# Kernel tuning notes

Hardware: AMD Instinct MI355X
Metric: run time of the kernel (lower is better)

The kernel has to match this reference:

```python
import jax, jax.numpy as jnp
import numpy as np
import math

HEADS = 16
DIMS = 1024
SEQ_LEN = 2048
RANK_K = 128
BATCH = 8


def setup_inputs() -> dict:
    key = jax.random.key(0)
    ks = jax.random.split(key, 14)
    dh_std = 1.0 / math.sqrt(DIMS)
    proj_std = 1.0 / math.sqrt(RANK_K)
    inp = {
        "q": jax.random.normal(ks[0], (BATCH, SEQ_LEN, DIMS), jnp.float32),
        "k": jax.random.normal(ks[1], (BATCH, SEQ_LEN, DIMS), jnp.float32),
        "v": jax.random.normal(ks[2], (BATCH, SEQ_LEN, DIMS), jnp.float32),
        # nn.Linear weights [out, in], bias [out]
        "Wq": jax.random.uniform(ks[3], (DIMS, DIMS), jnp.float32, -dh_std, dh_std),
        "bq": jax.random.uniform(ks[4], (DIMS,), jnp.float32, -dh_std, dh_std),
        "Wk": jax.random.uniform(ks[5], (DIMS, DIMS), jnp.float32, -dh_std, dh_std),
        "bk": jax.random.uniform(ks[6], (DIMS,), jnp.float32, -dh_std, dh_std),
        "Wv": jax.random.uniform(ks[7], (DIMS, DIMS), jnp.float32, -dh_std, dh_std),
        "bv": jax.random.uniform(ks[8], (DIMS,), jnp.float32, -dh_std, dh_std),
        # Linformer low-rank projections [seq_length, k], uniform(-1/sqrt(k), 1/sqrt(k))
        "proj_k": jax.random.uniform(ks[9], (SEQ_LEN, RANK_K), jnp.float32, -proj_std, proj_std),
        "proj_v": jax.random.uniform(ks[10], (SEQ_LEN, RANK_K), jnp.float32, -proj_std, proj_std),
        "Wo": jax.random.uniform(ks[11], (DIMS, DIMS), jnp.float32, -dh_std, dh_std),
        "bo": jax.random.uniform(ks[12], (DIMS,), jnp.float32, -dh_std, dh_std),
    }
    return inp


def reference(q, k, v, Wq, bq, Wk, bk, Wv, bv, proj_k, proj_v, Wo, bo):
    B, N, D = q.shape
    H = HEADS
    dh = D // H
    Kr = proj_k.shape[1]

    kp = k @ Wk.T + bk                       # [B, N, D]
    # faithful to original: plain reshape (view), NOT a head-split transpose
    qp = (q @ Wq.T + bq).reshape(B, H, N, dh)  # [B, H, N, dh]
    vp = v @ Wv.T + bv                       # [B, N, D]

    pk = jnp.einsum('bnd,nk->bkd', kp, proj_k[:N])  # [B, Kr, D]
    pv = jnp.einsum('bnd,nk->bkd', vp, proj_v[:N])  # [B, Kr, D]
    pk = pk.reshape(B, Kr, H, dh).transpose(0, 2, 1, 3)  # [B, H, Kr, dh]
    pv = pv.reshape(B, Kr, H, dh).transpose(0, 2, 1, 3)  # [B, H, Kr, dh]

    # scores [B,H,N,Kr] -> transposed to [B,H,Kr,N]; softmax over N (seq) axis
    scores = jnp.einsum('bhnd,bhkd->bhkn', qp, pk) / math.sqrt(dh)
    attn = jax.nn.softmax(scores, axis=-1)   # [B, H, Kr, N]
    out = jnp.einsum('bhkn,bhkd->bhnd', attn, pv)  # [B, H, N, dh]
    out = out.transpose(0, 2, 1, 3).reshape(B, N, D)
    return out @ Wo.T + bo
```

## Files before the change

kernel.cpp:

```cpp
#include <hip/hip_runtime.h>

typedef unsigned short u16;
typedef unsigned int   u32;
typedef __attribute__((ext_vector_type(4))) float fx4;
typedef __attribute__((ext_vector_type(8))) __bf16 bf16x8;
typedef __attribute__((ext_vector_type(8))) unsigned short us8;
typedef __attribute__((ext_vector_type(2))) unsigned int u32x2;

__device__ __forceinline__ u16 f2bf(float x){
  u32 u = __builtin_bit_cast(u32, x);
  u += 0x7fffu + ((u >> 16) & 1u);
  return (u16)(u >> 16);
}
__device__ __forceinline__ float b2f(u16 h){
  u32 u = ((u32)h) << 16;
  return __builtin_bit_cast(float, u);
}
__device__ __forceinline__ void gld16(const void* g, void* l){
  __builtin_amdgcn_global_load_lds(
      (const __attribute__((address_space(1))) u32*)g,
      (__attribute__((address_space(3))) u32*)l, 16, 0, 0);
}
__device__ __forceinline__ void xcd_remap(u32& bx, u32& by, u32& bz){
  u32 nx = gridDim.x, ny = gridDim.y, nz = gridDim.z;
  u32 nwg = nx * ny * nz;
  u32 orig = (blockIdx.z * ny + blockIdx.y) * nx + blockIdx.x;
  u32 lid = (orig & 7u) * (nwg >> 3) + (orig >> 3);
  bx = lid % nx;
  u32 rem = lid / nx;
  by = rem % ny;
  bz = rem / ny;
}

__global__ __launch_bounds__(256) void k_f2bf(const float* __restrict__ in,
                                              u16* __restrict__ out, int n8){
  int i = blockIdx.x * 256 + threadIdx.x;
  const int stride = gridDim.x * 256;
  for (; i < n8; i += stride){
    const float4* p = (const float4*)in + (long)i * 2;
    float4 a = p[0], b = p[1];
    us8 o = { f2bf(a.x), f2bf(a.y), f2bf(a.z), f2bf(a.w),
              f2bf(b.x), f2bf(b.y), f2bf(b.z), f2bf(b.w) };
    *((us8*)out + i) = o;
  }
}

__global__ __launch_bounds__(256) void k_f2bfW(const float* __restrict__ w0,
                                               const float* __restrict__ w1,
                                               const float* __restrict__ w2,
                                               const float* __restrict__ w3,
                                               u16* __restrict__ out){
  const float* src = blockIdx.y == 0 ? w0 : blockIdx.y == 1 ? w1 :
                     blockIdx.y == 2 ? w2 : w3;
  u16* dst = out + (long)blockIdx.y * 1048576;
  int i = blockIdx.x * 256 + threadIdx.x;
  const int stride = gridDim.x * 256;
  for (; i < 131072; i += stride){
    const float4* p = (const float4*)src + (long)i * 2;
    float4 a = p[0], b = p[1];
    us8 o = { f2bf(a.x), f2bf(a.y), f2bf(a.z), f2bf(a.w),
              f2bf(b.x), f2bf(b.y), f2bf(b.z), f2bf(b.w) };
    *((us8*)dst + i) = o;
  }
}

__global__ void k_zero(float* p, int n){
  int i = blockIdx.x * 256 + threadIdx.x;
  if (i < n) p[i] = 0.f;
}

__global__ __launch_bounds__(256) void k_tconv(const float* __restrict__ in,
                                               u16* __restrict__ out,
                                               int R, int C, long sIn, long sOut,
                                               float* __restrict__ colsum){
  in  += (long)blockIdx.z * sIn;
  out += (long)blockIdx.z * sOut;
  const int c0 = blockIdx.x * 64, r0 = blockIdx.y * 64;
  __shared__ u16 tile[64][66];
  __shared__ float red[256];
  const int t = threadIdx.x;
  const int cc = t & 63, wq = t >> 6;
  float part = 0.f;
  #pragma unroll
  for (int i = 0; i < 16; ++i){
    int rr = i * 4 + wq;
    float v = in[(long)(r0 + rr) * C + c0 + cc];
    tile[rr][cc] = f2bf(v);
    part += v;
  }
  if (colsum){
    red[t] = part;
    __syncthreads();
    if (t < 64){
      float s = red[t] + red[t + 64] + red[t + 128] + red[t + 192];
      atomicAdd(&colsum[c0 + t], s);
    }
  }
  __syncthreads();
  const int oc0 = t >> 5, jb = (t & 31) * 2;
  #pragma unroll
  for (int i = 0; i < 8; ++i){
    int oc = oc0 + i * 8;
    u32 pk2 = (u32)tile[jb][oc] | ((u32)tile[jb + 1][oc] << 16);
    *(u32*)(out + (long)(c0 + oc) * R + r0 + jb) = pk2;
  }
}

template<int BM, int BN, int MODE, int EPI, typename OutT>
__global__ __launch_bounds__(256) void k_gemm(
    const u16* __restrict__ A, int lda, long sAz,
    const u16* __restrict__ B, int ldb, long sBz,
    OutT* __restrict__ C, int ldc, long sCz,
    int K, const float* __restrict__ bias, const float* __restrict__ srow, float scale)
{
  constexpr int BK = 64;
  constexpr int FM = BM / 32, FN = BN / 32;
  __shared__ u16 ldsA[BM * BK];
  __shared__ u16 ldsB[BN * BK];
  u32 bx, by, bz;
  xcd_remap(bx, by, bz);
  const long z = bz;
  if constexpr (MODE == 0){ A += z * sAz; B += z * sBz; C += z * sCz; }
  const int t = threadIdx.x;
  const int lane = t & 63;
  const int w = t >> 6, wm = w >> 1, wn = w & 1;
  const int r15 = lane & 15, g = lane >> 4;
  const int m0 = by * BM, n0 = bx * BN;
  fx4 acc[FM][FN] = {};
  constexpr int CA = BM * BK / (8 * 256);
  constexpr int CB = BN * BK / (8 * 256);
  for (int kt = 0; kt < K; kt += BK){
    #pragma unroll
    for (int i = 0; i < CA; ++i){
      int ch = i * 256 + t, row = ch >> 3, cc = ch & 7;
      gld16(A + (long)(m0 + row) * lda + kt + cc * 8, (char*)ldsA + ch * 16);
    }
    #pragma unroll
    for (int i = 0; i < CB; ++i){
      int ch = i * 256 + t, row = ch >> 3, cc = ch & 7;
      gld16(B + (long)(n0 + row) * ldb + kt + cc * 8, (char*)ldsB + ch * 16);
    }
    __syncthreads();
    #pragma unroll
    for (int ks = 0; ks < 2; ++ks){
      bf16x8 af[FM], bfv[FN];
      #pragma unroll
      for (int mf = 0; mf < FM; ++mf)
        af[mf] = *(const bf16x8*)&ldsA[(wm * (BM/2) + mf * 16 + r15) * BK + ks * 32 + g * 8];
      #pragma unroll
      for (int nf = 0; nf < FN; ++nf)
        bfv[nf] = *(const bf16x8*)&ldsB[(wn * (BN/2) + nf * 16 + r15) * BK + ks * 32 + g * 8];
      #pragma unroll
      for (int mf = 0; mf < FM; ++mf)
        #pragma unroll
        for (int nf = 0; nf < FN; ++nf)
          acc[mf][nf] = __builtin_amdgcn_mfma_f32_16x16x32_bf16(af[mf], bfv[nf], acc[mf][nf], 0, 0, 0);
    }
    __syncthreads();
  }
  #pragma unroll
  for (int mf = 0; mf < FM; ++mf){
    #pragma unroll
    for (int nf = 0; nf < FN; ++nf){
      const int row0 = m0 + wm * (BM/2) + mf * 16 + g * 4;
      const int col  = n0 + wn * (BN/2) + nf * 16 + r15;
      float vv[4];
      #pragma unroll
      for (int r = 0; r < 4; ++r){
        float v = acc[mf][nf][r];
        if constexpr (EPI == 1) v += bias[col];
        if constexpr (EPI == 2) v = (v + srow[row0 + r] * bias[col]) * scale;
        if constexpr (EPI == 3) v = v + srow[row0 + r] * bias[col];
        vv[r] = v;
      }
      if constexpr (EPI == 3){
        u32 lo = (u32)f2bf(vv[0]) | ((u32)f2bf(vv[1]) << 16);
        u32 hi = (u32)f2bf(vv[2]) | ((u32)f2bf(vv[3]) << 16);
        u32x2 pk2 = { lo, hi };
        *(u32x2*)((u16*)C + (long)col * 128 + row0) = pk2;
      } else {
        #pragma unroll
        for (int r = 0; r < 4; ++r){
          if constexpr (sizeof(OutT) == 2) C[(long)(row0 + r) * ldc + col] = (OutT)f2bf(vv[r]);
          else                             C[(long)(row0 + r) * ldc + col] = (OutT)vv[r];
        }
      }
    }
  }
}

template<int EPI, typename OutT>
__global__ __launch_bounds__(512, 1) void k_gemm256(
    const u16* __restrict__ A, int lda,
    const u16* __restrict__ B, int ldb,
    OutT* __restrict__ C, int ldc,
    int K, const float* __restrict__ bias)
{
  constexpr int BM = 256, BN = 128, BK = 64;
  __shared__ u16 ldsA[3][BM * BK];
  __shared__ u16 ldsB[3][BN * BK];
  u32 bx, by, bz;
  xcd_remap(bx, by, bz);
  const int m0 = by * BM, n0 = bx * BN;
  const int t = threadIdx.x;
  const int lane = t & 63, w = t >> 6;
  const int wm = w >> 1, wn = w & 1;
  const int r15 = lane & 15, g = lane >> 4;
  const int NT = K >> 6;

  auto stageA = [&](int kt, int buf){
    #pragma unroll
    for (int j = 0; j < 4; ++j){
      int ch = j * 512 + t, row = ch >> 3, cc = ch & 7;
      gld16(A + (long)(m0 + row) * lda + kt + ((cc ^ (row & 7)) * 8),
            (char*)ldsA[buf] + ch * 16);
    }
  };
  auto stageB = [&](int kt, int buf){
    #pragma unroll
    for (int j = 0; j < 2; ++j){
      int ch = j * 512 + t, row = ch >> 3, cc = ch & 7;
      gld16(B + (long)(n0 + row) * ldb + kt + ((cc ^ (row & 7)) * 8),
            (char*)ldsB[buf] + ch * 16);
    }
  };

  stageA(0, 0); stageB(0, 0);
  if (NT > 1){
    stageA(BK, 1); stageB(BK, 1);
    asm volatile("s_waitcnt vmcnt(6)" ::: "memory");
  } else {
    asm volatile("s_waitcnt vmcnt(0)" ::: "memory");
  }
  __builtin_amdgcn_s_barrier();
  asm volatile("" ::: "memory");

  fx4 acc[4][4] = {};
  for (int tt = 0; tt < NT; ++tt){
    const u16* bA = ldsA[tt % 3];
    const u16* bB = ldsB[tt % 3];
    const int sbuf = (tt + 2) % 3;
    const bool pf = (tt + 2 < NT);
    bf16x8 af[2][4], bf[2][2];
    #pragma unroll
    for (int ks = 0; ks < 2; ++ks)
      #pragma unroll
      for (int mf = 0; mf < 4; ++mf)
        af[ks][mf] = *(const bf16x8*)((const char*)bA +
            (wm * 64 + mf * 16 + r15) * 128 + (((ks * 4 + g) ^ (r15 & 7)) * 16));
    #pragma unroll
    for (int ks = 0; ks < 2; ++ks)
      #pragma unroll
      for (int nf = 0; nf < 2; ++nf)
        bf[ks][nf] = *(const bf16x8*)((const char*)bB +
            (wn * 64 + nf * 16 + r15) * 128 + (((ks * 4 + g) ^ (r15 & 7)) * 16));
    if (pf) stageA((tt + 2) * BK, sbuf);
    asm volatile("" ::: "memory");
    __builtin_amdgcn_s_barrier();
    asm volatile("" ::: "memory");
    __builtin_amdgcn_s_setprio(1);
    #pragma unroll
    for (int ks = 0; ks < 2; ++ks)
      #pragma unroll
      for (int mf = 0; mf < 4; ++mf)
        #pragma unroll
        for (int nf = 0; nf < 2; ++nf)
          acc[mf][nf] = __builtin_amdgcn_mfma_f32_16x16x32_bf16(af[ks][mf], bf[ks][nf], acc[mf][nf], 0, 0, 0);
    __builtin_amdgcn_s_setprio(0);
    asm volatile("" ::: "memory");
    __builtin_amdgcn_s_barrier();
    asm volatile("" ::: "memory");
    bf16x8 bf2[2][2];
    #pragma unroll
    for (int ks = 0; ks < 2; ++ks)
      #pragma unroll
      for (int nf = 0; nf < 2; ++nf)
        bf2[ks][nf] = *(const bf16x8*)((const char*)bB +
            (wn * 64 + (nf + 2) * 16 + r15) * 128 + (((ks * 4 + g) ^ (r15 & 7)) * 16));
    if (pf) stageB((tt + 2) * BK, sbuf);
    __builtin_amdgcn_s_setprio(1);
    #pragma unroll
    for (int ks = 0; ks < 2; ++ks)
      #pragma unroll
      for (int mf = 0; mf < 4; ++mf)
        #pragma unroll
        for (int nf = 0; nf < 2; ++nf)
          acc[mf][nf + 2] = __builtin_amdgcn_mfma_f32_16x16x32_bf16(af[ks][mf], bf2[ks][nf], acc[mf][nf + 2], 0, 0, 0);
    __builtin_amdgcn_s_setprio(0);
    if (pf)                { asm volatile("s_waitcnt vmcnt(6)" ::: "memory"); }
    else if (tt + 1 < NT)  { asm volatile("s_waitcnt vmcnt(0)" ::: "memory"); }
    asm volatile("" ::: "memory");
    __builtin_amdgcn_s_barrier();
    asm volatile("" ::: "memory");
  }

  #pragma unroll
  for (int mf = 0; mf < 4; ++mf)
    #pragma unroll
    for (int nf = 0; nf < 4; ++nf){
      const int row0 = m0 + wm * 64 + mf * 16 + g * 4;
      const int col  = n0 + wn * 64 + nf * 16 + r15;
      float bcol = 0.f;
      if constexpr (EPI == 1) bcol = bias[col];
      #pragma unroll
      for (int r = 0; r < 4; ++r){
        float vv = acc[mf][nf][r] + bcol;
        if constexpr (sizeof(OutT) == 2) C[(long)(row0 + r) * ldc + col] = (OutT)f2bf(vv);
        else                             C[(long)(row0 + r) * ldc + col] = (OutT)vv;
      }
    }
}

__global__ __launch_bounds__(256) void k_gemmTN(
    const u16* __restrict__ projT, const float* __restrict__ ksrc,
    const float* __restrict__ vsrc, u16* __restrict__ ck)
{
  u32 bx, by, bz; xcd_remap(bx, by, bz);
  const int p = bz >> 3, b = bz & 7;
  const u16* A = projT + p * 262144;
  const float* S = (p ? vsrc : ksrc) + (long)b * 2097152;
  u16* C = ck + p * 1048576 + b * 131072;
  const int d0 = bx * 64;
  __shared__ u16 ldsA[128 * 64];
  __shared__ u16 ldsB[64 * 72];
  const int t = threadIdx.x, lane = t & 63, w = t >> 6;
  const int wm = w >> 1, wn = w & 1;
  const int r15 = lane & 15, g = lane >> 4;
  const int c4 = t & 15, r4 = t >> 4;
  fx4 acc[4][2] = {};
  for (int kt = 0; kt < 2048; kt += 64){
    #pragma unroll
    for (int i = 0; i < 4; ++i){
      int ch = i * 256 + t, row = ch >> 3, cc = ch & 7;
      gld16(A + (long)row * 2048 + kt + ((cc ^ (row & 7)) * 8), (char*)ldsA + ch * 16);
    }
    float4 f[4];
    #pragma unroll
    for (int i = 0; i < 4; ++i)
      f[i] = *(const float4*)(S + (long)(kt + r4 * 4 + i) * 1024 + d0 + c4 * 4);
    #pragma unroll
    for (int j = 0; j < 4; ++j){
      u32 lo = (u32)f2bf(((const float*)&f[0])[j]) | ((u32)f2bf(((const float*)&f[1])[j]) << 16);
      u32 hi = (u32)f2bf(((const float*)&f[2])[j]) | ((u32)f2bf(((const float*)&f[3])[j]) << 16);
      u32x2 pr = { lo, hi };
      *(u32x2*)&ldsB[(c4 * 4 + j) * 72 + r4 * 4] = pr;
    }
    __syncthreads();
    #pragma unroll
    for (int ks = 0; ks < 2; ++ks){
      bf16x8 af[4], bfv[2];
      #pragma unroll
      for (int mf = 0; mf < 4; ++mf){
        int row = wm * 64 + mf * 16 + r15;
        af[mf] = *(const bf16x8*)((const char*)ldsA + row * 128 + (((ks * 4 + g) ^ (row & 7)) * 16));
      }
      #pragma unroll
      for (int nf = 0; nf < 2; ++nf)
        bfv[nf] = *(const bf16x8*)&ldsB[(wn * 32 + nf * 16 + r15) * 72 + ks * 32 + g * 8];
      #pragma unroll
      for (int mf = 0; mf < 4; ++mf)
        #pragma unroll
        for (int nf = 0; nf < 2; ++nf)
          acc[mf][nf] = __builtin_amdgcn_mfma_f32_16x16x32_bf16(af[mf], bfv[nf], acc[mf][nf], 0, 0, 0);
    }
    __syncthreads();
  }
  #pragma unroll
  for (int mf = 0; mf < 4; ++mf)
    #pragma unroll
    for (int nf = 0; nf < 2; ++nf){
      const int row0 = wm * 64 + mf * 16 + g * 4;
      const int col  = d0 + wn * 32 + nf * 16 + r15;
      #pragma unroll
      for (int r = 0; r < 4; ++r)
        C[(long)(row0 + r) * 1024 + col] = f2bf(acc[mf][nf][r]);
    }
}

__global__ __launch_bounds__(512) void k_stats(const u16* __restrict__ pk,
                                               const u16* __restrict__ qp,
                                               float* __restrict__ invZ){
  const int z = blockIdx.x;
  const int b = z >> 4, h = z & 15;
  const u16* pkh = pk + b * 131072 + h * 64;
  const u16* qph = qp + (long)z * 131072;
  __shared__ u16 pkL[128 * 64];
  __shared__ float zred[8][128];
  const int t = threadIdx.x, lane = t & 63, w = t >> 6;
  const int r15 = lane & 15, g = lane >> 4;
  #pragma unroll
  for (int i = 0; i < 2; ++i){
    int ch = i * 512 + t, row = ch >> 3, cc = ch & 7;
    int csrc = cc ^ (row & 7);
    gld16(pkh + (long)row * 1024 + csrc * 8, (char*)pkL + ch * 16);
  }
  __syncthreads();
  float zacc[8][4] = {};
  for (int c = 0; c < 8; ++c){
    const int n0 = w * 256 + c * 32;
    fx4 acc[8][2] = {};
    #pragma unroll
    for (int ks = 0; ks < 2; ++ks){
      bf16x8 bq[2];
      #pragma unroll
      for (int nf = 0; nf < 2; ++nf)
        bq[nf] = *(const bf16x8*)(qph + (long)(n0 + nf * 16 + r15) * 64 + ks * 32 + g * 8);
      #pragma unroll
      for (int mf = 0; mf < 8; ++mf){
        int row = mf * 16 + r15;
        int x = (ks * 4 + g) ^ (row & 7);
        bf16x8 a = *(const bf16x8*)((const char*)pkL + row * 128 + x * 16);
        #pragma unroll
        for (int nf = 0; nf < 2; ++nf)
          acc[mf][nf] = __builtin_amdgcn_mfma_f32_16x16x32_bf16(a, bq[nf], acc[mf][nf], 0, 0, 0);
      }
    }
    #pragma unroll
    for (int mf = 0; mf < 8; ++mf)
      #pragma unroll
      for (int nf = 0; nf < 2; ++nf)
        #pragma unroll
        for (int r = 0; r < 4; ++r)
          zacc[mf][r] += __expf(acc[mf][nf][r]);
  }
  #pragma unroll
  for (int mf = 0; mf < 8; ++mf)
    #pragma unroll
    for (int r = 0; r < 4; ++r){
      float v = zacc[mf][r];
      v += __shfl_xor(v, 1); v += __shfl_xor(v, 2);
      v += __shfl_xor(v, 4); v += __shfl_xor(v, 8);
      zacc[mf][r] = v;
    }
  if (r15 == 0){
    #pragma unroll
    for (int mf = 0; mf < 8; ++mf)
      #pragma unroll
      for (int r = 0; r < 4; ++r)
        zred[w][mf * 16 + g * 4 + r] = zacc[mf][r];
  }
  __syncthreads();
  if (t < 128){
    float s = 0.f;
    #pragma unroll
    for (int w2 = 0; w2 < 8; ++w2) s += zred[w2][t];
    invZ[(long)z * 128 + t] = 1.0f / s;
  }
}

__global__ __launch_bounds__(256) void k_attn(const u16* __restrict__ pk,
                                              const u16* __restrict__ qp,
                                              const u16* __restrict__ pvT,
                                              const float* __restrict__ invZ,
                                              u16* __restrict__ outh){
  u32 bx, by, bz;
  xcd_remap(bx, by, bz);
  const int z = by, nb = bx;
  const int b = z >> 4, h = z & 15;
  const u16* pkh = pk  + b * 131072 + h * 64;
  const u16* qph = qp  + (long)z * 131072;
  const u16* pvh = pvT + b * 131072 + h * 8192;
  const float* zh = invZ + (long)z * 128;
  __shared__ u16 pkL[128 * 64];
  __shared__ u16 ptL[4][32 * 132];
  __shared__ float zL[128];
  const int t = threadIdx.x, lane = t & 63, w = t >> 6;
  const int r15 = lane & 15, g = lane >> 4;
  #pragma unroll
  for (int i = 0; i < 4; ++i){
    int ch = i * 256 + t, row = ch >> 3, cc = ch & 7;
    int csrc = cc ^ (row & 7);
    gld16(pkh + (long)row * 1024 + csrc * 8, (char*)pkL + ch * 16);
  }
  if (t < 128) zL[t] = zh[t];
  __syncthreads();
  const int n0 = nb * 128 + w * 32;
  fx4 acc[8][2] = {};
  #pragma unroll
  for (int ks = 0; ks < 2; ++ks){
    bf16x8 bq[2];
    #pragma unroll
    for (int nf = 0; nf < 2; ++nf)
      bq[nf] = *(const bf16x8*)(qph + (long)(n0 + nf * 16 + r15) * 64 + ks * 32 + g * 8);
    #pragma unroll
    for (int mf = 0; mf < 8; ++mf){
      int row = mf * 16 + r15;
      int x = (ks * 4 + g) ^ (row & 7);
      bf16x8 a = *(const bf16x8*)((const char*)pkL + row * 128 + x * 16);
      #pragma unroll
      for (int nf = 0; nf < 2; ++nf)
        acc[mf][nf] = __builtin_amdgcn_mfma_f32_16x16x32_bf16(a, bq[nf], acc[mf][nf], 0, 0, 0);
    }
  }
  u16* pt = ptL[w];
  #pragma unroll
  for (int mf = 0; mf < 8; ++mf){
    const int kb = mf * 16 + g * 4;
    const float z0 = zL[kb], z1 = zL[kb + 1], z2 = zL[kb + 2], z3 = zL[kb + 3];
    #pragma unroll
    for (int nf = 0; nf < 2; ++nf){
      const int nl = nf * 16 + r15;
      u32 lo = (u32)f2bf(__expf(acc[mf][nf][0]) * z0) |
               ((u32)f2bf(__expf(acc[mf][nf][1]) * z1) << 16);
      u32 hi = (u32)f2bf(__expf(acc[mf][nf][2]) * z2) |
               ((u32)f2bf(__expf(acc[mf][nf][3]) * z3) << 16);
      u32x2 pkd = { lo, hi };
      *(u32x2*)(pt + nl * 132 + kb) = pkd;
    }
  }
  fx4 o[2][4] = {};
  #pragma unroll
  for (int ks = 0; ks < 4; ++ks){
    bf16x8 bv[4];
    #pragma unroll
    for (int nf = 0; nf < 4; ++nf)
      bv[nf] = *(const bf16x8*)(pvh + (long)(nf * 16 + r15) * 128 + ks * 32 + g * 8);
    #pragma unroll
    for (int mf = 0; mf < 2; ++mf){
      bf16x8 pa = *(const bf16x8*)(pt + (mf * 16 + r15) * 132 + ks * 32 + g * 8);
      #pragma unroll
      for (int nf = 0; nf < 4; ++nf)
        o[mf][nf] = __builtin_amdgcn_mfma_f32_16x16x32_bf16(pa, bv[nf], o[mf][nf], 0, 0, 0);
    }
  }
  u16* og = outh + ((long)b * 2048 + n0) * 1024 + h * 64;
  #pragma unroll
  for (int mf = 0; mf < 2; ++mf)
    #pragma unroll
    for (int nf = 0; nf < 4; ++nf)
      #pragma unroll
      for (int r = 0; r < 4; ++r){
        int nl = mf * 16 + g * 4 + r;
        og[(long)nl * 1024 + nf * 16 + r15] = f2bf(o[mf][nf][r]);
      }
}

extern "C" void kernel_launch(void* const* d_in, const int* in_sizes, int n_in,
                              void* d_out, int out_size, void* d_ws, size_t ws_size,
                              hipStream_t stream)
{
  const float* q   = (const float*)d_in[0];
  const float* k   = (const float*)d_in[1];
  const float* v   = (const float*)d_in[2];
  const float* Wq  = (const float*)d_in[3];
  const float* bq  = (const float*)d_in[4];
  const float* Wk  = (const float*)d_in[5];
  const float* bk  = (const float*)d_in[6];
  const float* Wv  = (const float*)d_in[7];
  const float* bv  = (const float*)d_in[8];
  const float* pjk = (const float*)d_in[9];
  const float* pjv = (const float*)d_in[10];
  const float* Wo  = (const float*)d_in[11];
  const float* bo  = (const float*)d_in[12];

  if (ws_size < 152044544u) return;

  char* ws = (char*)d_ws;
  u16*  q_bf  = (u16*)(ws + 0);
  float* invZ = (float*)(ws + 33554432);
  u16*  W_bf  = (u16*)(ws + 100663296);
  u16*  projT = (u16*)(ws + 109051904);
  float* sk   = (float*)(ws + 110100480);
  float* sv   = (float*)(ws + 110100992);
  u16*  qp    = (u16*)(ws + 110101504);
  u16*  ck    = (u16*)(ws + 143655936);
  u16*  pk    = (u16*)(ws + 147850240);
  u16*  pvT   = (u16*)(ws + 149947392);
  u16*  outh  = (u16*)(ws + 0);
  u16*  Wq_bf = W_bf, *Wk_bf = W_bf + 1048576, *Wv_bf = W_bf + 2097152, *Wo_bf = W_bf + 3145728;

  k_zero<<<1, 256, 0, stream>>>(sk, 256);

  k_f2bf<<<2048, 256, 0, stream>>>(q, q_bf, 2097152);
  k_f2bfW<<<dim3(128,4), 256, 0, stream>>>(Wq, Wk, Wv, Wo, W_bf);
  k_tconv<<<dim3(2,32,1),  256, 0, stream>>>(pjk, projT,          2048, 128, 0, 0, sk);
  k_tconv<<<dim3(2,32,1),  256, 0, stream>>>(pjv, projT + 262144, 2048, 128, 0, 0, sv);

  k_gemm256<1,u16><<<dim3(8,64), 512, 0, stream>>>(
      q_bf,1024, Wq_bf,1024, qp,1024, 1024, bq);
  k_gemmTN<<<dim3(16,1,16), 256, 0, stream>>>(projT, k, v, ck);
  k_gemm<64,64,0,2,u16><<<dim3(16,2,8), 256, 0, stream>>>(
      ck,1024,131072, Wk_bf,1024,0, pk,1024,131072, 1024, bk, sk, 0.125f);
  k_gemm<64,64,0,3,u16><<<dim3(16,2,8), 256, 0, stream>>>(
      ck + 1048576,1024,131072, Wv_bf,1024,0, pvT,0,131072, 1024, bv, sv, 1.f);
  k_stats<<<128, 512, 0, stream>>>(pk, qp, invZ);
  k_attn<<<dim3(16,128), 256, 0, stream>>>(pk, qp, pvT, invZ, outh);
  k_gemm256<1,float><<<dim3(8,64), 512, 0, stream>>>(
      outh,1024, Wo_bf,1024, (float*)d_out,1024, 1024, bo);
}
```

Before: 250.4 us.

## Double-buffer gemmTN, split its M tile across blocks, fold zeroing into weight conversion

The projection GEMM (projT × k/v) now uses double-buffered LDS and prefetches the next K-tile of A and of the fp32 source while MFMAs run on the current tile. The 128-row M tile is split across two blocks via gridDim.y, which doubles the grid from 256 to 512 blocks for better CU occupancy but makes each block re-read and re-convert the fp32 k/v source. The separate k_zero launch is removed, and the column-sum buffer is instead zeroed by the first block of the weight-conversion kernel, saving one kernel launch.

```diff
diff --git a/kernel.cpp b/kernel.cpp
--- a/kernel.cpp
+++ b/kernel.cpp
@@ -49,7 +49,9 @@
                                                const float* __restrict__ w1,
                                                const float* __restrict__ w2,
                                                const float* __restrict__ w3,
-                                               u16* __restrict__ out){
+                                               u16* __restrict__ out,
+                                               float* __restrict__ zbuf){
+  if (blockIdx.x == 0 && blockIdx.y == 0) zbuf[threadIdx.x] = 0.f;
   const float* src = blockIdx.y == 0 ? w0 : blockIdx.y == 1 ? w1 :
                      blockIdx.y == 2 ? w2 : w3;
   u16* dst = out + (long)blockIdx.y * 1048576;
@@ -62,11 +64,6 @@
               f2bf(b.x), f2bf(b.y), f2bf(b.z), f2bf(b.w) };
     *((us8*)dst + i) = o;
   }
-}
-
-__global__ void k_zero(float* p, int n){
-  int i = blockIdx.x * 256 + threadIdx.x;
-  if (i < n) p[i] = 0.f;
 }
 
 __global__ __launch_bounds__(256) void k_tconv(const float* __restrict__ in,
@@ -317,59 +314,82 @@
 {
   u32 bx, by, bz; xcd_remap(bx, by, bz);
   const int p = bz >> 3, b = bz & 7;
-  const u16* A = projT + p * 262144;
+  const u16* A = projT + p * 262144 + by * 64 * 2048;
   const float* S = (p ? vsrc : ksrc) + (long)b * 2097152;
-  u16* C = ck + p * 1048576 + b * 131072;
+  u16* C = ck + p * 1048576 + b * 131072 + by * 64 * 1024;
   const int d0 = bx * 64;
-  __shared__ u16 ldsA[128 * 64];
-  __shared__ u16 ldsB[64 * 72];
+  __shared__ u16 ldsA[2][64 * 64];
+  __shared__ u16 ldsB[2][64 * 72];
   const int t = threadIdx.x, lane = t & 63, w = t >> 6;
   const int wm = w >> 1, wn = w & 1;
   const int r15 = lane & 15, g = lane >> 4;
   const int c4 = t & 15, r4 = t >> 4;
-  fx4 acc[4][2] = {};
-  for (int kt = 0; kt < 2048; kt += 64){
-    #pragma unroll
-    for (int i = 0; i < 4; ++i){
+
+  auto ldA = [&](int kt, int buf){
+    #pragma unroll
+    for (int i = 0; i < 2; ++i){
       int ch = i * 256 + t, row = ch >> 3, cc = ch & 7;
-      gld16(A + (long)row * 2048 + kt + ((cc ^ (row & 7)) * 8), (char*)ldsA + ch * 16);
-    }
-    float4 f[4];
+      gld16(A + (long)row * 2048 + kt + ((cc ^ (row & 7)) * 8),
+            (char*)ldsA[buf] + ch * 16);
+    }
+  };
+  auto ldS = [&](int kt, float4* f){
     #pragma unroll
     for (int i = 0; i < 4; ++i)
       f[i] = *(const float4*)(S + (long)(kt + r4 * 4 + i) * 1024 + d0 + c4 * 4);
+  };
+  auto wrB = [&](const float4* f, int buf){
     #pragma unroll
     for (int j = 0; j < 4; ++j){
       u32 lo = (u32)f2bf(((const float*)&f[0])[j]) | ((u32)f2bf(((const float*)&f[1])[j]) << 16);
       u32 hi = (u32)f2bf(((const float*)&f[2])[j]) | ((u32)f2bf(((const float*)&f[3])[j]) << 16);
       u32x2 pr = { lo, hi };
-      *(u32x2*)&ldsB[(c4 * 4 + j) * 72 + r4 * 4] = pr;
-    }
-    __syncthreads();
+      *(u32x2*)&ldsB[buf][(c4 * 4 + j) * 72 + r4 * 4] = pr;
+    }
+  };
+
+  { float4 f0[4];
+    ldS(0, f0); ldA(0, 0);
+    asm volatile("s_waitcnt vmcnt(0)" ::: "memory");
+    wrB(f0, 0); }
+  __syncthreads();
+
+  fx4 acc[2][2] = {};
+  for (int tt = 0; tt < 32; ++tt){
+    const int buf = tt & 1;
+    const bool pf = (tt + 1 < 32);
+    float4 fn[4];
+    if (pf){ ldS((tt + 1) * 64, fn); ldA((tt + 1) * 64, buf ^ 1); }
+    asm volatile("" ::: "memory");
     #pragma unroll
     for (int ks = 0; ks < 2; ++ks){
-      bf16x8 af[4], bfv[2];
-      #pragma unroll
-      for (int mf = 0; mf < 4; ++mf){
-        int row = wm * 64 + mf * 16 + r15;
-        af[mf] = *(const bf16x8*)((const char*)ldsA + row * 128 + (((ks * 4 + g) ^ (row & 7)) * 16));
+      bf16x8 af[2], bfv[2];
+      #pragma unroll
+      for (int mf = 0; mf < 2; ++mf){
+        int row = wm * 32 + mf * 16 + r15;
+        af[mf] = *(const bf16x8*)((const char*)ldsA[buf] + row * 128 +
+                                  (((ks * 4 + g) ^ (row & 7)) * 16));
       }
       #pragma unroll
       for (int nf = 0; nf < 2; ++nf)
-        bfv[nf] = *(const bf16x8*)&ldsB[(wn * 32 + nf * 16 + r15) * 72 + ks * 32 + g * 8];
-      #pragma unroll
-      for (int mf = 0; mf < 4; ++mf)
+        bfv[nf] = *(const bf16x8*)&ldsB[buf][(wn * 32 + nf * 16 + r15) * 72 + ks * 32 + g * 8];
+      #pragma unroll
+      for (int mf = 0; mf < 2; ++mf)
         #pragma unroll
         for (int nf = 0; nf < 2; ++nf)
           acc[mf][nf] = __builtin_amdgcn_mfma_f32_16x16x32_bf16(af[mf], bfv[nf], acc[mf][nf], 0, 0, 0);
     }
+    if (pf){
+      asm volatile("s_waitcnt vmcnt(0)" ::: "memory");
+      wrB(fn, buf ^ 1);
+    }
     __syncthreads();
   }
   #pragma unroll
-  for (int mf = 0; mf < 4; ++mf)
+  for (int mf = 0; mf < 2; ++mf)
     #pragma unroll
     for (int nf = 0; nf < 2; ++nf){
-      const int row0 = wm * 64 + mf * 16 + g * 4;
+      const int row0 = wm * 32 + mf * 16 + g * 4;
       const int col  = d0 + wn * 32 + nf * 16 + r15;
       #pragma unroll
       for (int r = 0; r < 4; ++r)
@@ -569,16 +589,14 @@
   u16*  outh  = (u16*)(ws + 0);
   u16*  Wq_bf = W_bf, *Wk_bf = W_bf + 1048576, *Wv_bf = W_bf + 2097152, *Wo_bf = W_bf + 3145728;
 
-  k_zero<<<1, 256, 0, stream>>>(sk, 256);
-
   k_f2bf<<<2048, 256, 0, stream>>>(q, q_bf, 2097152);
-  k_f2bfW<<<dim3(128,4), 256, 0, stream>>>(Wq, Wk, Wv, Wo, W_bf);
+  k_f2bfW<<<dim3(128,4), 256, 0, stream>>>(Wq, Wk, Wv, Wo, W_bf, sk);
   k_tconv<<<dim3(2,32,1),  256, 0, stream>>>(pjk, projT,          2048, 128, 0, 0, sk);
   k_tconv<<<dim3(2,32,1),  256, 0, stream>>>(pjv, projT + 262144, 2048, 128, 0, 0, sv);
 
   k_gemm256<1,u16><<<dim3(8,64), 512, 0, stream>>>(
       q_bf,1024, Wq_bf,1024, qp,1024, 1024, bq);
-  k_gemmTN<<<dim3(16,1,16), 256, 0, stream>>>(projT, k, v, ck);
+  k_gemmTN<<<dim3(16,2,16), 256, 0, stream>>>(projT, k, v, ck);
   k_gemm<64,64,0,2,u16><<<dim3(16,2,8), 256, 0, stream>>>(
       ck,1024,131072, Wk_bf,1024,0, pk,1024,131072, 1024, bk, sk, 0.125f);
   k_gemm<64,64,0,3,u16><<<dim3(16,2,8), 256, 0, stream>>>(
```

Result: faster. 240.3 us (-4.0%).
